# Kernel optimization log

Measured on AMD Instinct MI355X. Metric: run time of the kernel, lower is better.

Reference implementation:

```python
import jax, jax.numpy as jnp
import numpy as np

PS = 3        # patch_size
RATE = 2      # rate
FS = 3        # fuse_kernel_size
SS = 10.0     # softmax_scale
PAD = (PS - 1) // 2       # tl.calc_padding(ps, 1)
FUSE_PAD = (FS - 1) // 2  # tl.calc_padding(fs, 1)
EPS = 1e-4


def extract_patches(x, ps, stride, pad):
    """x: (B,C,H,W) -> (B, L, C, ps, ps); L row-major over output positions (== F.unfold order)."""
    B, C, H, W = x.shape
    xp = jnp.pad(x, ((0, 0), (0, 0), (pad, pad), (pad, pad)))
    oh = (H + 2 * pad - ps) // stride + 1
    ow = (W + 2 * pad - ps) // stride + 1
    rows = []
    for dy in range(ps):  # small fixed loop (ps=3)
        cols = []
        for dx in range(ps):
            cols.append(xp[:, :, dy:dy + (oh - 1) * stride + 1:stride,
                              dx:dx + (ow - 1) * stride + 1:stride])
        rows.append(jnp.stack(cols, axis=2))           # (B,C,ps,oh,ow)
    p = jnp.stack(rows, axis=2)                        # (B,C,ps,ps,oh,ow)
    return p.reshape(B, C, ps, ps, oh * ow).transpose(0, 4, 1, 2, 3)


def diag_fuse(S, fs, pad):
    """conv2d of (N,N) 'image' with identity fs x fs kernel (diagonal smoothing)."""
    N = S.shape[0]
    Sp = jnp.pad(S, ((pad, pad), (pad, pad)))
    out = Sp[0:N, 0:N]
    for k in range(1, fs):  # fs=3, tiny fixed loop
        out = out + Sp[k:k + N, k:k + N]
    return out


def fuse_scores(S, hr, wr):
    L = hr * wr
    S = diag_fuse(S, FS, FUSE_PAD)
    S = S.reshape(hr, wr, hr, wr).transpose(1, 0, 3, 2).reshape(L, L)
    S = diag_fuse(S, FS, FUSE_PAD)
    S = S.reshape(wr, hr, wr, hr).transpose(1, 0, 3, 2).reshape(L, L)
    return S


def contextual_attention(f_o, b_o, mask_o):
    B, c, h, w = f_o.shape
    # nearest downsample by 1/rate == strided slice
    f = f_o[:, :, ::RATE, ::RATE]
    b = b_o[:, :, ::RATE, ::RATE]
    m = mask_o[:, :, ::RATE, ::RATE]
    hr, wr = f.shape[2], f.shape[3]
    L = hr * wr

    fg = extract_patches(f, PS, 1, PAD)        # (B,L,c,ps,ps) foreground neighborhoods
    bs = extract_patches(b, PS, 1, PAD)        # (B,L,c,ps,ps) shrunk bg patches
    bi = extract_patches(b_o, PS, RATE, PAD)   # (B,L,c,ps,ps) full-res bg patches

    bnorm = jnp.maximum(jnp.sqrt(jnp.sum(bs * bs, axis=(2, 3, 4))), EPS)  # (B,L)
    bsn = bs / bnorm[:, :, None, None, None]

    # score[b,p,q] = <normalized bg patch p, fg neighborhood at position q>
    S = jnp.einsum('bpcij,bqcij->bpq', bsn, fg)  # (B,L,L)
    S = jax.vmap(lambda s: fuse_scores(s, hr, wr))(S)

    # valid-patch indicator from downsampled mask
    mp = extract_patches(m, PS, 1, PAD)                                   # (B,L,1,ps,ps)
    valid = (jnp.mean(mp, axis=(2, 3, 4)) == 0.0).astype(f_o.dtype)       # (B,L)

    score = S.reshape(B, L, hr, wr) * valid[:, :, None, None]
    score = jax.nn.softmax(score * SS, axis=1) * valid[:, :, None, None]

    # conv_transpose2d(score, bi, stride=RATE, padding=PAD, output_padding=1) / 4
    wgt = jnp.flip(bi.transpose(0, 2, 1, 3, 4), axis=(-2, -1))  # (B,c,L,ps,ps)
    pad_cfg = [(PS - 1 - PAD, PS - 1 - PAD + 1)] * 2            # output_padding on high side

    def agg(s, wk):  # s:(L,hr,wr), wk:(c,L,ps,ps)
        return jax.lax.conv_general_dilated(
            s[None], wk, (1, 1), pad_cfg, lhs_dilation=(RATE, RATE),
            dimension_numbers=('NCHW', 'OIHW', 'NCHW'))[0]

    out = jax.vmap(agg)(score, wgt) / 4.0   # (B,c,h,w)
    return out


def setup_inputs() -> dict:
    key = jax.random.key(0)
    k1, k2, k3 = jax.random.split(key, 3)
    f_o = jax.random.normal(k1, (16, 128, 64, 64), dtype=jnp.float32)
    b_o = jax.random.normal(k2, (16, 128, 64, 64), dtype=jnp.float32)
    mask_o = jax.random.randint(k3, (16, 1, 64, 64), 0, 2).astype(jnp.float32)
    return {"f_o": f_o, "b_o": b_o, "mask_o": mask_o}


def reference(f_o, b_o, mask_o):
    return contextual_attention(f_o, b_o, mask_o)
```

## Files before the change

### kernel.cpp

```cpp
#include <hip/hip_runtime.h>
#include <cmath>

#define CC 128
#define HH 64
#define WWI 64
#define LL 1024
#define NB 16
#define MM 1152
#define KC 384
#define TPD 1156

#define SLAB      2977808ul
#define OFF_TP    0
#define OFF_S3T   0
#define OFF_W     0
#define OFF_S2    1336336
#define OFF_SCORET 1336336
#define OFF_POOL  2384912
#define OFF_N2    2974736
#define OFF_BNORM 2975760
#define OFF_VALID 2976784

#define NHROW 132
#define NH1 (NHROW * TPD)
#define NHALO (NH1 + 1024 * NHROW)
#define ZCHK ((NHALO + 255) / 256)

typedef __bf16 bf16x8 __attribute__((ext_vector_type(8)));
typedef __bf16 bf16x4 __attribute__((ext_vector_type(4)));
typedef float f32x4 __attribute__((ext_vector_type(4)));

#define GLDS(g, l) __builtin_amdgcn_global_load_lds( \
    (const __attribute__((address_space(1))) unsigned int*)(const void*)(g), \
    (__attribute__((address_space(3))) unsigned int*)(void*)(l), 16, 0, 0)


__global__ __launch_bounds__(256) void k_prep(const float* __restrict__ f_o,
                                              const float* __restrict__ b_o,
                                              float* __restrict__ ws,
                                              int b0, int aff) {
    int bz, uy;
    if (aff) { int g = blockIdx.x; bz = g & 15; uy = g >> 4; }
    else     { bz = blockIdx.y; uy = blockIdx.x; }
    int gb = b0 + bz;
    __shared__ float lf[128 * 33];
    __shared__ float lb[128 * 33];
    __shared__ float red[8 * 32];
    int tid = threadIdx.x;
    int ux = tid & 31, co = tid >> 5;
    size_t pix = (size_t)(2 * uy) * WWI + 2 * ux;
    const float* fbp = f_o + (size_t)gb * CC * HH * WWI + pix;
    const float* bbp = b_o + (size_t)gb * CC * HH * WWI + pix;
#pragma unroll
    for (int pass = 0; pass < 16; pass++) {
        int c = pass * 8 + co;
        lf[c * 33 + ux] = fbp[(size_t)c * HH * WWI];
        lb[c * 33 + ux] = bbp[(size_t)c * HH * WWI];
    }
    __syncthreads();
    int ux2 = tid >> 3, cg = (tid & 7) * 16;
    int u = uy * 32 + ux2;
    __bf16* bcat = (__bf16*)(ws + (size_t)bz * SLAB + OFF_POOL) + (size_t)u * KC;
    __bf16* fcat = bcat + 393216;
    float s2 = 0.f;
#pragma unroll
    for (int k = 0; k < 16; k++) {
        int c = cg + k;
        float fv = lf[c * 33 + ux2];
        float bv = lb[c * 33 + ux2];
        __bf16 fhi = (__bf16)fv; __bf16 flo = (__bf16)(fv - (float)fhi);
        __bf16 bhi = (__bf16)bv; __bf16 blo = (__bf16)(bv - (float)bhi);
        bcat[c] = bhi; bcat[128 + c] = bhi; bcat[256 + c] = blo;
        fcat[c] = fhi; fcat[128 + c] = flo; fcat[256 + c] = fhi;
        s2 += bv * bv;
    }
    red[(tid & 7) * 32 + ux2] = s2;
    __syncthreads();
    if (tid < 32) {
        float s = 0.f;
#pragma unroll
        for (int k = 0; k < 8; k++) s += red[k * 32 + tid];
        ws[(size_t)bz * SLAB + OFF_N2 + uy * 32 + tid] = s;
    }
}

__global__ __launch_bounds__(256) void k_bnorm_valid(float* __restrict__ ws,
                                                     const float* __restrict__ mask,
                                                     int b0, int aff) {
    int g = blockIdx.x;
    int bz, pc;
    if (aff) { bz = g & 15; pc = g >> 4; }
    else     { bz = g >> 2; pc = g & 3; }
    int p = pc * 256 + threadIdx.x;
    int gb = b0 + bz;
    int py = p >> 5, px = p & 31;
    const float* mb = mask + (size_t)gb * HH * WWI;
    const float* n2 = ws + (size_t)bz * SLAB + OFF_N2;
    float s = 0.f, msum = 0.f;
#pragma unroll
    for (int dy = -1; dy <= 1; dy++) {
#pragma unroll
        for (int dx = -1; dx <= 1; dx++) {
            int py2 = py + dy, px2 = px + dx;
            if ((unsigned)py2 < 32u && (unsigned)px2 < 32u) {
                s    += n2[(py2 << 5) | px2];
                msum += mb[(2 * py2) * WWI + 2 * px2];
            }
        }
    }
    ws[(size_t)bz * SLAB + OFF_BNORM + p] = fmaxf(sqrtf(s), 1e-4f);
    ws[(size_t)bz * SLAB + OFF_VALID + p] = (msum == 0.0f) ? 1.0f : 0.0f;
}

__device__ __forceinline__ int halo_idx(int k) {
    if (k < 34) return k;
    if (k < 68) return 1122 + (k - 34);
    if (k < 100) return 34 * (k - 100 + 33);
    return 34 * (k - 132 + 33) + 33;
}

__global__ __launch_bounds__(256) void k_zerohalo(float* __restrict__ ws, int aff) {
    int bz, t;
    if (aff) { int g = blockIdx.x; bz = g & 15; t = (g >> 4) * 256 + threadIdx.x; }
    else     { bz = blockIdx.y; t = blockIdx.x * 256 + threadIdx.x; }
    if (t >= NHALO) return;
    float* Tp = ws + (size_t)bz * SLAB + OFF_TP;
    if (t < NH1) {
        int R = halo_idx(t / TPD);
        Tp[(size_t)R * TPD + (t % TPD)] = 0.f;
    } else {
        int t2 = t - NH1;
        int ir = t2 / NHROW;
        int R  = 34 * (1 + (ir >> 5)) + 1 + (ir & 31);
        int C  = halo_idx(t2 % NHROW);
        Tp[(size_t)R * TPD + C] = 0.f;
    }
}

template<int KTOT>
__device__ __forceinline__ void gemm_core(const __bf16* __restrict__ Ab,
                                          const __bf16* __restrict__ Bb,
                                          int lda, int ldb, int m0, int n0,
                                          __bf16* As, __bf16* Bs,
                                          f32x4 acc[4][4]) {
    int t = threadIdx.x;
    int lane = t & 63, w = t >> 6;
    int rsub = lane >> 3;
    int g8   = ((lane & 7) ^ (rsub & 7)) * 8;
    int lm = lane & 15, kgf = lane >> 4;
    int wm = (w & 1) * 64, wn = (w >> 1) * 64;

#define ISSUE(kt, buf) do {                                                   \
    int k0_ = (kt) * 64;                                                      \
    _Pragma("unroll")                                                         \
    for (int ci = 0; ci < 4; ci++) {                                          \
        int rb = ci * 32 + w * 8;                                             \
        int r  = rb + rsub;                                                   \
        GLDS(Ab + (size_t)(m0 + r) * lda + k0_ + g8, &As[(buf) + rb * 64]);   \
        GLDS(Bb + (size_t)(n0 + r) * ldb + k0_ + g8, &Bs[(buf) + rb * 64]);   \
    } } while (0)

#define COMPUTE(curoff) do {                                                  \
    _Pragma("unroll")                                                         \
    for (int s2 = 0; s2 < 2; s2++) {                                          \
        bf16x8 af[4], bfr[4];                                                 \
        _Pragma("unroll")                                                     \
        for (int i = 0; i < 4; i++)                                           \
            af[i] = *(const bf16x8*)&As[(curoff) + (wm + i * 16 + lm) * 64 +  \
                                        (((s2 * 4 + kgf) ^ (lm & 7)) * 8)];   \
        _Pragma("unroll")                                                     \
        for (int j = 0; j < 4; j++)                                           \
            bfr[j] = *(const bf16x8*)&Bs[(curoff) + (wn + j * 16 + lm) * 64 + \
                                         (((s2 * 4 + kgf) ^ (lm & 7)) * 8)];  \
        _Pragma("unroll")                                                     \
        for (int i = 0; i < 4; i++)                                           \
            _Pragma("unroll")                                                 \
            for (int j = 0; j < 4; j++)                                       \
                acc[i][j] = __builtin_amdgcn_mfma_f32_16x16x32_bf16(          \
                    af[i], bfr[j], acc[i][j], 0, 0, 0);                       \
    } } while (0)

    const int NIT = KTOT / 64;

    ISSUE(0, 0);
    ISSUE(1, 8192);

#pragma unroll 2
    for (int it = 0; it < NIT - 2; it++) {
        int cur = (it & 1) * 8192;
        asm volatile("s_waitcnt vmcnt(8)" ::: "memory");
        __builtin_amdgcn_sched_barrier(0);
        __builtin_amdgcn_s_barrier();
        COMPUTE(cur);
        __builtin_amdgcn_s_barrier();
        ISSUE(it + 2, cur);
    }
    asm volatile("s_waitcnt vmcnt(8)" ::: "memory");
    __builtin_amdgcn_sched_barrier(0);
    __builtin_amdgcn_s_barrier();
    COMPUTE(((NIT - 2) & 1) * 8192);
    __builtin_amdgcn_s_barrier();
    asm volatile("s_waitcnt vmcnt(0)" ::: "memory");
    __builtin_amdgcn_sched_barrier(0);
    __builtin_amdgcn_s_barrier();
    COMPUTE(((NIT - 1) & 1) * 8192);

#undef ISSUE
#undef COMPUTE
}

__global__ __launch_bounds__(256) void k_gemm_T_mfma(float* __restrict__ ws, int swz) {
    int bz, m0, n0;
    if (swz) {
        bz = blockIdx.x + 8 * (blockIdx.z & 1);
        m0 = blockIdx.y * 128;
        n0 = (blockIdx.z >> 1) * 128;
    } else {
        bz = blockIdx.z; m0 = blockIdx.y * 128; n0 = blockIdx.x * 128;
    }
    const __bf16* Ab = (const __bf16*)(ws + (size_t)bz * SLAB + OFF_POOL);
    const __bf16* Bb = Ab + 393216;
    float* Tp = ws + (size_t)bz * SLAB + OFF_TP;
    __shared__ __align__(16) __bf16 As[2 * 128 * 64];
    __shared__ __align__(16) __bf16 Bs[2 * 128 * 64];
    f32x4 acc[4][4];
#pragma unroll
    for (int i = 0; i < 4; i++)
#pragma unroll
        for (int j = 0; j < 4; j++) acc[i][j] = (f32x4)0.0f;
    gemm_core<KC>(Ab, Bb, KC, KC, m0, n0, As, Bs, acc);
    int lane = threadIdx.x & 63, w = threadIdx.x >> 6;
    int lm = lane & 15, kgf = lane >> 4;
    int wm = (w & 1) * 64, wn = (w >> 1) * 64;
#pragma unroll
    for (int i = 0; i < 4; i++) {
#pragma unroll
        for (int r = 0; r < 4; r++) {
            int m = m0 + wm + i * 16 + kgf * 4 + r;
            float* dst = Tp + (size_t)(((m >> 5) + 1) * 34 + (m & 31) + 1) * TPD;
#pragma unroll
            for (int j = 0; j < 4; j++) {
                int v = n0 + wn + j * 16 + lm;
                dst[((v >> 5) + 1) * 34 + (v & 31) + 1] = acc[i][j][r];
            }
        }
    }
}

__global__ __launch_bounds__(512, 2) void k_gemm_W192(float* __restrict__ ws) {
    int d = blockIdx.x;
    int c = d & 7, s = d >> 3;
    int bz  = c + 8 * (s / 24);
    int t24 = s % 24;
    int m0 = (t24 >> 2) * 192;
    int n0 = (t24 & 3) * 256;
    const __bf16* Ab = (const __bf16*)(ws + (size_t)bz * SLAB + OFF_POOL);
    const __bf16* Bb = (const __bf16*)(ws + (size_t)bz * SLAB + OFF_SCORET);
    __bf16* Wb = (__bf16*)(ws + (size_t)bz * SLAB + OFF_W);
    __shared__ __align__(16) __bf16 As[2 * 192 * 64];
    __shared__ __align__(16) __bf16 Bs[2 * 256 * 64];

    int t = threadIdx.x;
    int lane = t & 63, w = t >> 6;
    int rsub = lane >> 3;
    int g8   = ((lane & 7) ^ (rsub & 7)) * 8;
    int lm = lane & 15, kgf = lane >> 4;
    int wr = (w >> 2) * 96;
    int wc = (w & 3) * 64;

    f32x4 acc[6][4];
#pragma unroll
    for (int i = 0; i < 6; i++)
#pragma unroll
        for (int j = 0; j < 4; j++) acc[i][j] = (f32x4)0.0f;

#define WSTAGE(nbA, nbB, k1_) do {                                            \
    _Pragma("unroll")                                                         \
    for (int ci = 0; ci < 3; ci++) {                                          \
        int rb = ci * 64 + w * 8;                                             \
        GLDS(Ab + (size_t)(m0 + rb + rsub) * LL + (k1_) + g8,                 \
             &As[(nbA) + rb * 64]);                                           \
    }                                                                         \
    _Pragma("unroll")                                                         \
    for (int ci = 0; ci < 4; ci++) {                                          \
        int rb = ci * 64 + w * 8;                                             \
        GLDS(Bb + (size_t)(n0 + rb + rsub) * LL + (k1_) + g8,                 \
             &Bs[(nbB) + rb * 64]);                                           \
    } } while (0)

#define RD_A(mh, boA) do {                                                    \
    _Pragma("unroll")                                                         \
    for (int mi = 0; mi < 3; mi++)                                            \
        _Pragma("unroll")                                                     \
        for (int ks = 0; ks < 2; ks++)                                        \
            af[mi][ks] = *(const bf16x8*)&As[(boA) +                          \
                (wr + (mh) * 48 + mi * 16 + lm) * 64 +                        \
                (((ks * 4 + kgf) ^ (lm & 7)) * 8)];                           \
    } while (0)

#define RD_B(njlo, boB) do {                                                  \
    _Pragma("unroll")                                                         \
    for (int nj = 0; nj < 2; nj++)                                            \
        _Pragma("unroll")                                                     \
        for (int ks = 0; ks < 2; ks++)                                        \
            bfr[(njlo) + nj][ks] = *(const bf16x8*)&Bs[(boB) +                \
                (wc + ((njlo) + nj) * 16 + lm) * 64 +                         \
                (((ks * 4 + kgf) ^ (lm & 7)) * 8)];                           \
    } while (0)

#define QMFMA(mb, njlo) do {                                                  \
    __builtin_amdgcn_s_setprio(1);                                            \
    _Pragma("unroll")                                                         \
    for (int ks = 0; ks < 2; ks++)                                            \
        _Pragma("unroll")                                                     \
        for (int mi = 0; mi < 3; mi++)                                        \
            _Pragma("unroll")                                                 \
            for (int nj = 0; nj < 2; nj++)                                    \
                acc[(mb) + mi][(njlo) + nj] =                                 \
                    __builtin_amdgcn_mfma_f32_16x16x32_bf16(                  \
                        af[mi][ks], bfr[(njlo) + nj][ks],                     \
                        acc[(mb) + mi][(njlo) + nj], 0, 0, 0);                \
    __builtin_amdgcn_s_setprio(0);                                            \
    } while (0)

    WSTAGE(0, 0, 0);
    asm volatile("s_waitcnt vmcnt(0)" ::: "memory");
    __builtin_amdgcn_sched_barrier(0);
    __builtin_amdgcn_s_barrier();

#pragma unroll 2
    for (int kt = 0; kt < 16; kt++) {
        int boA = (kt & 1) * 12288, boB = (kt & 1) * 16384;
        int nbA = boA ^ 12288, nbB = boB ^ 16384;
        bf16x8 af[3][2], bfr[4][2];
        if (kt < 15) WSTAGE(nbA, nbB, (kt + 1) * 64);
        RD_A(0, boA);
        RD_B(0, boB);
        QMFMA(0, 0);
        RD_B(2, boB);
        QMFMA(0, 2);
        RD_A(1, boA);
        QMFMA(3, 2);
        QMFMA(3, 0);
        if (kt < 15) {
            asm volatile("s_waitcnt vmcnt(0)" ::: "memory");
            __builtin_amdgcn_sched_barrier(0);
            __builtin_amdgcn_s_barrier();
        }
    }

#undef WSTAGE
#undef RD_A
#undef RD_B
#undef QMFMA

#pragma unroll
    for (int mf = 0; mf < 6; mf++) {
#pragma unroll
        for (int r = 0; r < 4; r++) {
            int m = m0 + wr + mf * 16 + kgf * 4 + r;
            __bf16* dst = Wb + (size_t)m * LL + n0 + wc + lm;
#pragma unroll
            for (int nj = 0; nj < 4; nj++)
                dst[nj * 16] = (__bf16)acc[mf][nj][r];
        }
    }
}

__global__ __launch_bounds__(256) void k_gemm_W_mfma(float* __restrict__ ws, int swz) {
    int bz, m0, n0;
    if (swz) {
        bz = blockIdx.x + 8 * (blockIdx.z & 1);
        m0 = blockIdx.y * 128;
        n0 = (blockIdx.z >> 1) * 128;
    } else {
        bz = blockIdx.z; m0 = blockIdx.y * 128; n0 = blockIdx.x * 128;
    }
    const __bf16* Ab = (const __bf16*)(ws + (size_t)bz * SLAB + OFF_POOL);
    const __bf16* Bb = (const __bf16*)(ws + (size_t)bz * SLAB + OFF_SCORET);
    __bf16* Wb = (__bf16*)(ws + (size_t)bz * SLAB + OFF_W);
    __shared__ __align__(16) __bf16 As[2 * 128 * 64];
    __shared__ __align__(16) __bf16 Bs[2 * 128 * 64];
    f32x4 acc[4][4];
#pragma unroll
    for (int i = 0; i < 4; i++)
#pragma unroll
        for (int j = 0; j < 4; j++) acc[i][j] = (f32x4)0.0f;
    gemm_core<LL>(Ab, Bb, LL, LL, m0, n0, As, Bs, acc);
    int lane = threadIdx.x & 63, w = threadIdx.x >> 6;
    int lm = lane & 15, kgf = lane >> 4;
    int wm = (w & 1) * 64, wn = (w >> 1) * 64;
#pragma unroll
    for (int i = 0; i < 4; i++) {
#pragma unroll
        for (int r = 0; r < 4; r++) {
            int m = m0 + wm + i * 16 + kgf * 4 + r;
            __bf16* dst = Wb + (size_t)m * LL + n0 + wn + lm;
#pragma unroll
            for (int j = 0; j < 4; j++)
                dst[j * 16] = (__bf16)acc[i][j][r];
        }
    }
}

__global__ __launch_bounds__(256) void k_s12(float* __restrict__ ws, int aff) {
    int bz, i0;
    if (aff) { int g = blockIdx.x; bz = g & 15; i0 = (g >> 4) * 8; }
    else     { bz = blockIdx.y; i0 = blockIdx.x * 8; }
    const float* Tp = ws + (size_t)bz * SLAB + OFF_TP;
    const float* bn = ws + (size_t)bz * SLAB + OFF_BNORM;
    float* S2 = ws + (size_t)bz * SLAB + OFF_S2;
    __shared__ float Dsh[10][1024];
    int tid = threadIdx.x;
    for (int rl = 0; rl < 10; rl++) {
        int r = i0 - 1 + rl;
        if ((unsigned)r >= 1024u) continue;
        float invr = 1.0f / bn[r];
        size_t rbase = (size_t)(((r >> 5) + 1) * 34 + (r & 31) + 1) * TPD;
#pragma unroll
        for (int so = 0; so < 4; so++) {
            int s = so * 256 + tid;
            const float* cb = Tp + rbase + ((s >> 5) + 1) * 34 + (s & 31) + 1;
            float d = 0.f;
#pragma unroll
            for (int dy = -1; dy <= 1; dy++)
#pragma unroll
                for (int dx = -1; dx <= 1; dx++)
                    d += cb[dy * (34 * TPD + 34) + dx * (TPD + 1)];
            Dsh[rl][s] = d * invr;
        }
    }
    __syncthreads();
#pragma unroll
    for (int il = 0; il < 8; il++) {
        int i = i0 + il;
        float* orow = S2 + (size_t)i * LL;
#pragma unroll
        for (int jo = 0; jo < 4; jo++) {
            int j = jo * 256 + tid;
            float acc = 0.f;
#pragma unroll
            for (int k1 = -1; k1 <= 1; k1++) {
                int r = i + k1, s = j + k1;
                if ((unsigned)r < 1024u && (unsigned)s < 1024u)
                    acc += Dsh[il + 1 + k1][s];
            }
            orow[j] = acc;
        }
    }
}

__global__ __launch_bounds__(256) void k_st3t(float* __restrict__ ws, int aff) {
    int bz, p0, q0;
    if (aff) {
        int g = blockIdx.x; bz = g & 15;
        int tile = g >> 4; p0 = (tile >> 4) * 64; q0 = (tile & 15) * 64;
    } else {
        bz = blockIdx.z; p0 = blockIdx.y * 64; q0 = blockIdx.x * 64;
    }
    const float* ib = ws + (size_t)bz * SLAB + OFF_S2;
    float* ob = ws + (size_t)bz * SLAB + OFF_S3T;
    __shared__ float tile[64][65];
    int t = threadIdx.x;
#pragma unroll
    for (int it = 0; it < 16; it++) {
        int e = it * 256 + t;
        int pl = e >> 6, ql = e & 63;
        int p = p0 + pl, q = q0 + ql;
        int sp = ((p & 31) << 5) | (p >> 5);
        int sq = ((q & 31) << 5) | (q >> 5);
        float acc = 0.f;
#pragma unroll
        for (int k = -1; k <= 1; k++) {
            int tp = sp + k, tq = sq + k;
            if ((unsigned)tp < 1024u && (unsigned)tq < 1024u) {
                int row = ((tp & 31) << 5) | (tp >> 5);
                int col = ((tq & 31) << 5) | (tq >> 5);
                acc += ib[(size_t)row * LL + col];
            }
        }
        tile[pl][ql] = acc;
    }
    __syncthreads();
#pragma unroll
    for (int it = 0; it < 16; it++) {
        int e = it * 256 + t;
        int ql = e >> 6, pl = e & 63;
        ob[(size_t)(q0 + ql) * LL + p0 + pl] = tile[pl][ql];
    }
}

__global__ __launch_bounds__(256) void k_softmax_bf(float* __restrict__ ws, int aff) {
    int bz, q;
    if (aff) {
        int g = blockIdx.x; bz = g & 15;
        q = (g >> 4) * 4 + (threadIdx.x >> 6);
    } else {
        bz = blockIdx.z;
        q = blockIdx.x * 4 + (threadIdx.x >> 6);
    }
    int lane = threadIdx.x & 63;
    const float* row = ws + (size_t)bz * SLAB + OFF_S3T + (size_t)q * LL;
    const float* vb  = ws + (size_t)bz * SLAB + OFF_VALID;
    __bf16* orow = (__bf16*)(ws + (size_t)bz * SLAB + OFF_SCORET) + (size_t)q * LL;

    float4 v[4], vl[4];
#pragma unroll
    for (int i = 0; i < 4; i++) {
        int p = lane * 4 + i * 256;
        float4 s = *(const float4*)(row + p);
        float4 m = *(const float4*)(vb + p);
        v[i] = {s.x * m.x, s.y * m.y, s.z * m.z, s.w * m.w};
        vl[i] = m;
    }
    float mx = -1e30f;
#pragma unroll
    for (int i = 0; i < 4; i++)
        mx = fmaxf(mx, fmaxf(fmaxf(v[i].x, v[i].y), fmaxf(v[i].z, v[i].w)));
#pragma unroll
    for (int k = 1; k < 64; k <<= 1)
        mx = fmaxf(mx, __shfl_xor(mx, k, 64));
    float sum = 0.f;
    float4 e[4];
#pragma unroll
    for (int i = 0; i < 4; i++) {
        e[i].x = __expf(10.f * (v[i].x - mx));
        e[i].y = __expf(10.f * (v[i].y - mx));
        e[i].z = __expf(10.f * (v[i].z - mx));
        e[i].w = __expf(10.f * (v[i].w - mx));
        sum += e[i].x + e[i].y + e[i].z + e[i].w;
    }
#pragma unroll
    for (int k = 1; k < 64; k <<= 1)
        sum += __shfl_xor(sum, k, 64);
    float inv = 1.0f / sum;
#pragma unroll
    for (int i = 0; i < 4; i++) {
        bf16x4 o;
        o[0] = (__bf16)(e[i].x * inv * vl[i].x);
        o[1] = (__bf16)(e[i].y * inv * vl[i].y);
        o[2] = (__bf16)(e[i].z * inv * vl[i].z);
        o[3] = (__bf16)(e[i].w * inv * vl[i].w);
        *(bf16x4*)(orow + lane * 4 + i * 256) = o;
    }
}

__global__ __launch_bounds__(256) void k_makeA(const float* __restrict__ b_o,
                                               float* __restrict__ ws,
                                               int b0, int aff) {
    int c, bz;
    if (aff) { int g = blockIdx.x; bz = g & 15; c = g >> 4; }
    else     { c = blockIdx.x; bz = blockIdx.y; }
    int gb = b0 + bz;
    __shared__ float img[64][65];
    int t = threadIdx.x;
    const float4* src = (const float4*)(b_o + (size_t)(gb * CC + c) * HH * WWI);
#pragma unroll
    for (int it = 0; it < 4; it++) {
        int idx = it * 256 + t;
        float4 v = src[idx];
        int row = idx >> 4, col4 = (idx & 15) * 4;
        img[row][col4] = v.x; img[row][col4 + 1] = v.y;
        img[row][col4 + 2] = v.z; img[row][col4 + 3] = v.w;
    }
    __syncthreads();
    __bf16* Ab = (__bf16*)(ws + (size_t)bz * SLAB + OFF_POOL) + (size_t)c * 9 * LL;
    int py = t >> 3, px4 = (t & 7) * 4;
#pragma unroll
    for (int jy = 0; jy < 3; jy++) {
        int row = 2 * py + jy - 1;
        bool rok = (unsigned)row < 64u;
#pragma unroll
        for (int jx = 0; jx < 3; jx++) {
            bf16x4 o;
#pragma unroll
            for (int e = 0; e < 4; e++) {
                int col = 2 * (px4 + e) + jx - 1;
                float v = (rok && (unsigned)col < 64u) ? img[rok ? row : 0][(unsigned)col < 64u ? col : 0] : 0.f;
                o[e] = (__bf16)v;
            }
            *(bf16x4*)(Ab + (size_t)(jy * 3 + jx) * LL + t * 4) = o;
        }
    }
}

__global__ __launch_bounds__(256) void k_gather(const float* __restrict__ ws,
                                                float* __restrict__ outp,
                                                int b0, int aff) {
    int t;
    if (aff) {
        int g = blockIdx.x;
        int bz_ = g & 15;
        t = (bz_ << 19) + (g >> 4) * 256 + threadIdx.x;
    } else {
        t = blockIdx.x * 256 + threadIdx.x;
    }
    int ox = t & 63, oy = (t >> 6) & 63, c = (t >> 12) & 127, bz = t >> 19;
    const __bf16* Wb = (const __bf16*)(ws + (size_t)bz * SLAB + OFF_W);
    int qyA = (oy + 1) >> 1;
    int jyA = (oy & 1) ? 0 : 1;
    int vA  = (qyA < 32);
    int qyB = (oy - 1) >> 1;
    int vB  = (oy & 1);
    int qxA = (ox + 1) >> 1;
    int jxA = (ox & 1) ? 0 : 1;
    int uA  = (qxA < 32);
    int qxB = (ox - 1) >> 1;
    int uB  = (ox & 1);
    const __bf16* base = Wb + (size_t)c * 9 * LL;
    float s = 0.f;
    if (vA && uA) s += (float)base[(size_t)(jyA * 3 + jxA) * LL + qyA * 32 + qxA];
    if (vA && uB) s += (float)base[(size_t)(jyA * 3 + 2)   * LL + qyA * 32 + qxB];
    if (vB && uA) s += (float)base[(size_t)(2 * 3 + jxA)   * LL + qyB * 32 + qxA];
    if (vB && uB) s += (float)base[(size_t)(2 * 3 + 2)     * LL + qyB * 32 + qxB];
    outp[((size_t)((b0 + bz) * CC + c) * HH + oy) * WWI + ox] = 0.25f * s;
}

extern "C" void kernel_launch(void* const* d_in, const int* in_sizes, int n_in,
                              void* d_out, int out_size, void* d_ws, size_t ws_size,
                              hipStream_t stream) {
    (void)in_sizes; (void)n_in; (void)out_size;
    const float* f_o  = (const float*)d_in[0];
    const float* b_o  = (const float*)d_in[1];
    const float* mask = (const float*)d_in[2];
    float* out = (float*)d_out;

    int G = (int)(ws_size / (SLAB * sizeof(float)));
    if (G < 1) G = 1;
    if (G > NB) G = NB;
    float* ws = (float*)d_ws;

    for (int b0 = 0; b0 < NB; b0 += G) {
        int Gc = NB - b0 < G ? NB - b0 : G;
        if (Gc == NB) {
            k_prep<<<dim3(512), 256, 0, stream>>>(f_o, b_o, ws, 0, 1);
            k_bnorm_valid<<<dim3(64), 256, 0, stream>>>(ws, mask, 0, 1);
            k_zerohalo<<<dim3(16 * ZCHK), 256, 0, stream>>>(ws, 1);
            k_gemm_T_mfma<<<dim3(8, 8, 16), 256, 0, stream>>>(ws, 1);
            k_s12<<<dim3(2048), 256, 0, stream>>>(ws, 1);
            k_st3t<<<dim3(4096), 256, 0, stream>>>(ws, 1);
            k_softmax_bf<<<dim3(4096), 256, 0, stream>>>(ws, 1);
            k_makeA<<<dim3(2048), 256, 0, stream>>>(b_o, ws, 0, 1);
            k_gemm_W192<<<dim3(384), 512, 0, stream>>>(ws);
            k_gather<<<dim3(32768), 256, 0, stream>>>(ws, out, 0, 1);
        } else {
            k_prep<<<dim3(32, Gc), 256, 0, stream>>>(f_o, b_o, ws, b0, 0);
            k_bnorm_valid<<<dim3(Gc * 4), 256, 0, stream>>>(ws, mask, b0, 0);
            k_zerohalo<<<dim3(ZCHK, Gc), 256, 0, stream>>>(ws, 0);
            k_gemm_T_mfma<<<dim3(Gc, 8, 8), 256, 0, stream>>>(ws, 0);
            k_s12<<<dim3(128, Gc), 256, 0, stream>>>(ws, 0);
            k_st3t<<<dim3(16, 16, Gc), 256, 0, stream>>>(ws, 0);
            k_softmax_bf<<<dim3(256, 1, Gc), 256, 0, stream>>>(ws, 0);
            k_makeA<<<dim3(CC, Gc), 256, 0, stream>>>(b_o, ws, b0, 0);
            k_gemm_W_mfma<<<dim3(8, 9, Gc), 256, 0, stream>>>(ws, 0);
            k_gather<<<dim3(Gc * 2048), 256, 0, stream>>>(ws, out, b0, 0);
        }
    }
}
```

Before: 356.1 us.

## Store GEMM scores densely and replace zeroed halo with bounds checks

The score matrix T was stored in a padded 34x34-by-34x34 layout (stride 1156) whose halo had to be zeroed by a separate kernel. The GEMM now writes a dense 1024x1024 matrix, k_zerohalo is removed, and k_s12 handles borders with explicit bounds checks on the 3x3 neighbourhood. This removes one launch and its scattered zeroing writes and gives contiguous GEMM stores, at the cost of branchy address arithmetic in the stencil. The W192 grid-to-tile mapping is also reordered so each group of 8 consecutive blocks spreads across different batches differently.

After: 448.4 us. 25.9% more time.

```diff
diff --git a/kernel.cpp b/kernel.cpp
--- a/kernel.cpp
+++ b/kernel.cpp
@@ -8,7 +8,6 @@
 #define NB 16
 #define MM 1152
 #define KC 384
-#define TPD 1156
 
 #define SLAB      2977808ul
 #define OFF_TP    0
@@ -21,11 +20,6 @@
 #define OFF_BNORM 2975760
 #define OFF_VALID 2976784
 
-#define NHROW 132
-#define NH1 (NHROW * TPD)
-#define NHALO (NH1 + 1024 * NHROW)
-#define ZCHK ((NHALO + 255) / 256)
-
 typedef __bf16 bf16x8 __attribute__((ext_vector_type(8)));
 typedef __bf16 bf16x4 __attribute__((ext_vector_type(4)));
 typedef float f32x4 __attribute__((ext_vector_type(4)));
@@ -33,7 +27,6 @@
 #define GLDS(g, l) __builtin_amdgcn_global_load_lds( \
     (const __attribute__((address_space(1))) unsigned int*)(const void*)(g), \
     (__attribute__((address_space(3))) unsigned int*)(void*)(l), 16, 0, 0)
-
 
 __global__ __launch_bounds__(256) void k_prep(const float* __restrict__ f_o,
                                               const float* __restrict__ b_o,
@@ -110,31 +103,6 @@
     }
     ws[(size_t)bz * SLAB + OFF_BNORM + p] = fmaxf(sqrtf(s), 1e-4f);
     ws[(size_t)bz * SLAB + OFF_VALID + p] = (msum == 0.0f) ? 1.0f : 0.0f;
-}
-
-__device__ __forceinline__ int halo_idx(int k) {
-    if (k < 34) return k;
-    if (k < 68) return 1122 + (k - 34);
-    if (k < 100) return 34 * (k - 100 + 33);
-    return 34 * (k - 132 + 33) + 33;
-}
-
-__global__ __launch_bounds__(256) void k_zerohalo(float* __restrict__ ws, int aff) {
-    int bz, t;
-    if (aff) { int g = blockIdx.x; bz = g & 15; t = (g >> 4) * 256 + threadIdx.x; }
-    else     { bz = blockIdx.y; t = blockIdx.x * 256 + threadIdx.x; }
-    if (t >= NHALO) return;
-    float* Tp = ws + (size_t)bz * SLAB + OFF_TP;
-    if (t < NH1) {
-        int R = halo_idx(t / TPD);
-        Tp[(size_t)R * TPD + (t % TPD)] = 0.f;
-    } else {
-        int t2 = t - NH1;
-        int ir = t2 / NHROW;
-        int R  = 34 * (1 + (ir >> 5)) + 1 + (ir & 31);
-        int C  = halo_idx(t2 % NHROW);
-        Tp[(size_t)R * TPD + C] = 0.f;
-    }
 }
 
 template<int KTOT>
@@ -237,21 +205,19 @@
 #pragma unroll
         for (int r = 0; r < 4; r++) {
             int m = m0 + wm + i * 16 + kgf * 4 + r;
-            float* dst = Tp + (size_t)(((m >> 5) + 1) * 34 + (m & 31) + 1) * TPD;
-#pragma unroll
-            for (int j = 0; j < 4; j++) {
-                int v = n0 + wn + j * 16 + lm;
-                dst[((v >> 5) + 1) * 34 + (v & 31) + 1] = acc[i][j][r];
-            }
+            float* dst = Tp + (size_t)m * LL + n0 + wn + lm;
+#pragma unroll
+            for (int j = 0; j < 4; j++)
+                dst[j * 16] = acc[i][j][r];
         }
     }
 }
 
 __global__ __launch_bounds__(512, 2) void k_gemm_W192(float* __restrict__ ws) {
     int d = blockIdx.x;
-    int c = d & 7, s = d >> 3;
-    int bz  = c + 8 * (s / 24);
-    int t24 = s % 24;
+    int logical = (d & 7) * 48 + (d >> 3);
+    int bz  = logical / 24;
+    int t24 = logical % 24;
     int m0 = (t24 >> 2) * 192;
     int n0 = (t24 & 3) * 256;
     const __bf16* Ab = (const __bf16*)(ws + (size_t)bz * SLAB + OFF_POOL);
@@ -416,17 +382,20 @@
         int r = i0 - 1 + rl;
         if ((unsigned)r >= 1024u) continue;
         float invr = 1.0f / bn[r];
-        size_t rbase = (size_t)(((r >> 5) + 1) * 34 + (r & 31) + 1) * TPD;
+        int ry = r & 31, rb2 = r >> 5;
 #pragma unroll
         for (int so = 0; so < 4; so++) {
             int s = so * 256 + tid;
-            const float* cb = Tp + rbase + ((s >> 5) + 1) * 34 + (s & 31) + 1;
+            int sy = s & 31, sb2 = s >> 5;
             float d = 0.f;
 #pragma unroll
             for (int dy = -1; dy <= 1; dy++)
 #pragma unroll
-                for (int dx = -1; dx <= 1; dx++)
-                    d += cb[dy * (34 * TPD + 34) + dx * (TPD + 1)];
+                for (int dx = -1; dx <= 1; dx++) {
+                    if ((unsigned)(ry + dx) < 32u && (unsigned)(rb2 + dy) < 32u &&
+                        (unsigned)(sy + dx) < 32u && (unsigned)(sb2 + dy) < 32u)
+                        d += Tp[(size_t)(r + dy * 32 + dx) * LL + (s + dy * 32 + dx)];
+                }
             Dsh[rl][s] = d * invr;
         }
     }
@@ -635,7 +604,6 @@
         if (Gc == NB) {
             k_prep<<<dim3(512), 256, 0, stream>>>(f_o, b_o, ws, 0, 1);
             k_bnorm_valid<<<dim3(64), 256, 0, stream>>>(ws, mask, 0, 1);
-            k_zerohalo<<<dim3(16 * ZCHK), 256, 0, stream>>>(ws, 1);
             k_gemm_T_mfma<<<dim3(8, 8, 16), 256, 0, stream>>>(ws, 1);
             k_s12<<<dim3(2048), 256, 0, stream>>>(ws, 1);
             k_st3t<<<dim3(4096), 256, 0, stream>>>(ws, 1);
@@ -646,7 +614,6 @@
         } else {
             k_prep<<<dim3(32, Gc), 256, 0, stream>>>(f_o, b_o, ws, b0, 0);
             k_bnorm_valid<<<dim3(Gc * 4), 256, 0, stream>>>(ws, mask, b0, 0);
-            k_zerohalo<<<dim3(ZCHK, Gc), 256, 0, stream>>>(ws, 0);
             k_gemm_T_mfma<<<dim3(Gc, 8, 8), 256, 0, stream>>>(ws, 0);
             k_s12<<<dim3(128, Gc), 256, 0, stream>>>(ws, 0);
             k_st3t<<<dim3(16, 16, Gc), 256, 0, stream>>>(ws, 0);
```
